# Kernel tuning notes

Measured on AMD Instinct MI355X. Metric: run time of the kernel, lower is better.

The kernel has to match this reference:

```python
import jax, jax.numpy as jnp
import numpy as np

B, T, I, H = 256, 512, 300, 128


def setup_inputs() -> dict:
    key = jax.random.key(0)
    ks = jax.random.split(key, 7)
    s_ih = 1.0 / np.sqrt(H)
    return {
        "x": jax.random.normal(ks[0], (B, T, I), dtype=jnp.float32),
        # PyTorch LSTM params, gate order i,f,g,o stacked along first axis
        "W_ih": jax.random.uniform(ks[1], (4 * H, I), minval=-s_ih, maxval=s_ih, dtype=jnp.float32),
        "W_hh": jax.random.uniform(ks[2], (4 * H, H), minval=-s_ih, maxval=s_ih, dtype=jnp.float32),
        "b_ih": jax.random.uniform(ks[3], (4 * H,), minval=-s_ih, maxval=s_ih, dtype=jnp.float32),
        "b_hh": jax.random.uniform(ks[4], (4 * H,), minval=-s_ih, maxval=s_ih, dtype=jnp.float32),
        "fc_w": jax.random.uniform(ks[5], (1, H), minval=-s_ih, maxval=s_ih, dtype=jnp.float32),
        "fc_b": jax.random.uniform(ks[6], (1,), minval=-s_ih, maxval=s_ih, dtype=jnp.float32),
    }


def _lstm_last_h(x, W_ih, W_hh, b_ih, b_hh):
    # Precompute input contributions for all timesteps at once: [B,T,4H]
    xg = jnp.einsum("bti,gi->btg", x, W_ih) + b_ih + b_hh
    xg = jnp.transpose(xg, (1, 0, 2))  # [T,B,4H] for scan

    def step(carry, xg_t):
        h, c = carry
        gates = xg_t + h @ W_hh.T  # [B,4H]
        i, f, g, o = jnp.split(gates, 4, axis=-1)
        i = jax.nn.sigmoid(i)
        f = jax.nn.sigmoid(f)
        g = jnp.tanh(g)
        o = jax.nn.sigmoid(o)
        c = f * c + i * g
        h = o * jnp.tanh(c)
        return (h, c), None

    h0 = jnp.zeros((x.shape[0], W_hh.shape[1]), dtype=x.dtype)
    (h_last, _), _ = jax.lax.scan(step, (h0, h0), xg)
    return h_last  # [B,H]


def reference(x, W_ih, W_hh, b_ih, b_hh, fc_w, fc_b):
    h_last = _lstm_last_h(x, W_ih, W_hh, b_ih, b_hh)
    return h_last @ fc_w.T + fc_b  # [B,1]
```

## Files before the change

kernel.cpp:

```cpp
#include <hip/hip_runtime.h>
#include <cstdint>
#include <cstddef>

#define Bb   256
#define Tt   512
#define Ii   300
#define Hh   128
#define G4   512
#define KP   320

typedef _Float16 h2v   __attribute__((ext_vector_type(2)));
typedef _Float16 half8 __attribute__((ext_vector_type(8)));
typedef float    f32x4 __attribute__((ext_vector_type(4)));

typedef __attribute__((address_space(3))) unsigned int lds_uint;
typedef const __attribute__((address_space(1))) unsigned int glb_uint;

static __device__ __forceinline__ h2v as_h2(unsigned int u){ union{unsigned int u; h2v h;} c; c.u=u; return c.h; }
static __device__ __forceinline__ unsigned int as_u32(h2v h){ union{unsigned int u; h2v h;} c; c.h=h; return c.u; }

#if __has_builtin(__builtin_amdgcn_fdot2)
#define FDOT2(a,b,c) __builtin_amdgcn_fdot2((a),(b),(c),false)
#else
static __device__ __forceinline__ float FDOT2(h2v a, h2v b, float c){
  return c + (float)a[0]*(float)b[0] + (float)a[1]*(float)b[1];
}
#endif

__global__ __launch_bounds__(256) void conv_x(const float* __restrict__ x, unsigned int* __restrict__ x16){
  int idx = blockIdx.x*256 + threadIdx.x;
  int r   = idx / 160;
  int kk2 = idx - r*160;
  int kk  = kk2*2;
  const float* xr = x + (size_t)r*Ii;
  float v0 = (kk   < Ii) ? xr[kk]   : 0.f;
  float v1 = (kk+1 < Ii) ? xr[kk+1] : 0.f;
  h2v h; h[0] = (_Float16)v0; h[1] = (_Float16)v1;
  x16[idx] = as_u32(h);
}

__global__ __launch_bounds__(256) void conv_small(const float* __restrict__ Wih, const float* __restrict__ Whh,
      const float* __restrict__ bih, const float* __restrict__ bhh,
      unsigned int* __restrict__ W16, unsigned int* __restrict__ Whh2, float* __restrict__ bias){
  int idx = blockIdx.x*256 + threadIdx.x;
  if (idx < G4*160){
    int r = idx/160, kk2 = idx - r*160, kk = kk2*2;
    const float* wr = Wih + (size_t)r*Ii;
    float v0 = (kk   < Ii) ? wr[kk]   : 0.f;
    float v1 = (kk+1 < Ii) ? wr[kk+1] : 0.f;
    h2v h; h[0]=(_Float16)v0; h[1]=(_Float16)v1;
    W16[idx] = as_u32(h);
  } else if (idx < G4*160 + G4*64){
    int t = idx - G4*160; int j = t>>6, kk = t&63;
    float v0 = Whh[j*Hh + kk*2], v1 = Whh[j*Hh + kk*2 + 1];
    h2v h; h[0]=(_Float16)v0; h[1]=(_Float16)v1;
    Whh2[t] = as_u32(h);
  } else if (idx < G4*160 + G4*64 + G4){
    int d = idx - (G4*160 + G4*64);
    bias[d] = bih[d] + bhh[d];
  }
}

__global__ __launch_bounds__(256,2) void gemm16(const _Float16* __restrict__ A, const _Float16* __restrict__ Bm,
       const float* __restrict__ bias, float* __restrict__ C){
  __shared__ __align__(16) _Float16 As[128*32];
  __shared__ __align__(16) _Float16 Bs[128*32];
  int tid = threadIdx.x;
  int w = tid>>6, lane = tid&63;
  int bm = blockIdx.x*128, bn = blockIdx.y*128;
  f32x4 acc[2][8];
  #pragma unroll
  for (int i=0;i<2;i++)
    #pragma unroll
    for (int j=0;j<8;j++) acc[i][j] = (f32x4){0.f,0.f,0.f,0.f};

  int L0 = w*128 + lane, L1 = L0 + 64;
  int r0 = L0>>2, c0 = (L0&3) ^ (r0&3);
  int r1 = L1>>2, c1 = (L1&3) ^ (r1&3);
  const _Float16* gA0 = A  + (size_t)(bm+r0)*KP + c0*8;
  const _Float16* gA1 = A  + (size_t)(bm+r1)*KP + c1*8;
  const _Float16* gB0 = Bm + (size_t)(bn+r0)*KP + c0*8;
  const _Float16* gB1 = Bm + (size_t)(bn+r1)*KP + c1*8;

  int q = lane>>4, mr = lane&15;
  int m0 = w*32;
  int ra0 = m0+mr, ra1 = m0+16+mr;
  int oa0 = ra0*32 + ((q ^ (ra0&3))*8);
  int oa1 = ra1*32 + ((q ^ (ra1&3))*8);
  int ob[8];
  #pragma unroll
  for (int j=0;j<8;j++){ int rb = j*16+mr; ob[j] = rb*32 + ((q ^ (rb&3))*8); }

  for (int kt=0; kt<KP/32; ++kt){
    __syncthreads();
    __builtin_amdgcn_global_load_lds((glb_uint*)gA0, (lds_uint*)&As[w*1024      ], 16, 0, 0);
    __builtin_amdgcn_global_load_lds((glb_uint*)gA1, (lds_uint*)&As[w*1024 + 512], 16, 0, 0);
    __builtin_amdgcn_global_load_lds((glb_uint*)gB0, (lds_uint*)&Bs[w*1024      ], 16, 0, 0);
    __builtin_amdgcn_global_load_lds((glb_uint*)gB1, (lds_uint*)&Bs[w*1024 + 512], 16, 0, 0);
    gA0 += 32; gA1 += 32; gB0 += 32; gB1 += 32;
    __syncthreads();
    half8 af0 = *(const half8*)&As[oa0];
    half8 af1 = *(const half8*)&As[oa1];
    #pragma unroll
    for (int j=0;j<8;j++){
      half8 bf = *(const half8*)&Bs[ob[j]];
      acc[0][j] = __builtin_amdgcn_mfma_f32_16x16x32_f16(af0, bf, acc[0][j], 0,0,0);
      acc[1][j] = __builtin_amdgcn_mfma_f32_16x16x32_f16(af1, bf, acc[1][j], 0,0,0);
    }
  }
  #pragma unroll
  for (int j=0;j<8;j++){
    int gc = bn + j*16 + mr;
    float bv = bias[gc];
    #pragma unroll
    for (int i=0;i<2;i++){
      int gr0 = bm + w*32 + i*16 + q*4;
      #pragma unroll
      for (int reg=0; reg<4; ++reg)
        C[(size_t)(gr0+reg)*G4 + gc] = acc[i][j][reg] + bv;
    }
  }
}

__global__ __launch_bounds__(512,2) void lstm_rec(const float* __restrict__ xg, const unsigned int* __restrict__ Whh2,
     const float* __restrict__ fcw, const float* __restrict__ fcb, float* __restrict__ out){
  int tid = threadIdx.x;
  int b = blockIdx.x;
  int d = tid & 127;
  h2v w[64];
  #pragma unroll
  for (int k=0; k<64; ++k) w[k] = as_h2(Whh2[tid*64 + k]);

  __shared__ __align__(16) unsigned short hsh[128];
  __shared__ float gsh[512];
  __shared__ __align__(16) float xbuf[2][16*G4];
  if (tid < 64) ((unsigned int*)hsh)[tid] = 0;

  const float* xrow = xg + (size_t)b * (Tt*G4);
  int wv = tid >> 6, lane = tid & 63;

  auto stage = [&](int c){
    const float* src = xrow + (size_t)c*16*G4;
    float* dst = xbuf[c & 1];
    #pragma unroll
    for (int i=0; i<4; ++i){
      int off = i*2048 + wv*256;
      __builtin_amdgcn_global_load_lds((glb_uint*)(src + off + lane*4),
                                       (lds_uint*)(dst + off), 16, 0, 0);
    }
  };

  stage(0);
  float creg = 0.f, hreg = 0.f;
  __syncthreads();

  for (int t=0; t<Tt; ++t){
    if ((t & 15) == 0){
      int nc = (t >> 4) + 1;
      if (nc < Tt/16) stage(nc);
    }
    float xv = xbuf[(t >> 4) & 1][(t & 15)*G4 + tid];
    float a0 = 0.f, a1 = 0.f;
    const uint4* hv = (const uint4*)hsh;
    #pragma unroll
    for (int kq=0; kq<8; ++kq){
      uint4 hq0 = hv[kq*2], hq1 = hv[kq*2+1];
      a0 = FDOT2(as_h2(hq0.x), w[kq*8+0], a0); a1 = FDOT2(as_h2(hq0.y), w[kq*8+1], a1);
      a0 = FDOT2(as_h2(hq0.z), w[kq*8+2], a0); a1 = FDOT2(as_h2(hq0.w), w[kq*8+3], a1);
      a0 = FDOT2(as_h2(hq1.x), w[kq*8+4], a0); a1 = FDOT2(as_h2(hq1.y), w[kq*8+5], a1);
      a0 = FDOT2(as_h2(hq1.z), w[kq*8+6], a0); a1 = FDOT2(as_h2(hq1.w), w[kq*8+7], a1);
    }
    float a = a0 + a1 + xv;
    float act;
    if ((tid >> 7) == 2){ float e = __expf(2.f*a); act = 1.f - 2.f/(e+1.f); }
    else                { act = 1.f/(1.f+__expf(-a)); }
    gsh[tid] = act;
    __syncthreads();
    float gi = gsh[d], gf = gsh[128+d], gg = gsh[256+d], go = gsh[384+d];
    creg = gf*creg + gi*gg;
    float ec = __expf(2.f*creg); float tc = 1.f - 2.f/(ec+1.f);
    hreg = go*tc;
    if (tid < 128){
      union{ _Float16 f; unsigned short u; } cv; cv.f = (_Float16)hreg;
      hsh[tid] = cv.u;
    }
    __syncthreads();
  }

  if (tid < 128) gsh[tid] = hreg * fcw[tid];
  __syncthreads();
  if (tid < 64){
    float s = gsh[tid] + gsh[tid+64];
    #pragma unroll
    for (int st=32; st>=1; st>>=1) s += __shfl_down(s, st, 64);
    if (tid == 0) out[b] = s + fcb[0];
  }
}

extern "C" void kernel_launch(void* const* d_in, const int* in_sizes, int n_in,
                              void* d_out, int out_size, void* d_ws, size_t ws_size,
                              hipStream_t stream){
  const float* x   = (const float*)d_in[0];
  const float* Wih = (const float*)d_in[1];
  const float* Whh = (const float*)d_in[2];
  const float* bih = (const float*)d_in[3];
  const float* bhh = (const float*)d_in[4];
  const float* fcw = (const float*)d_in[5];
  const float* fcb = (const float*)d_in[6];
  float* out = (float*)d_out;
  char* ws = (char*)d_ws;

  unsigned int* x16   = (unsigned int*)(ws);
  unsigned int* W16   = (unsigned int*)(ws + 83886080);
  unsigned int* Whh2w = (unsigned int*)(ws + 84213760);
  float*        bias  = (float*)      (ws + 84344832);
  float*        xg    = (float*)      (ws + 84346880);

  hipLaunchKernelGGL(conv_x,     dim3(81920),  dim3(256), 0, stream, x, x16);
  hipLaunchKernelGGL(conv_small, dim3(450),    dim3(256), 0, stream, Wih, Whh, bih, bhh, W16, Whh2w, bias);
  hipLaunchKernelGGL(gemm16,     dim3(1024,4), dim3(256), 0, stream,
                     (const _Float16*)x16, (const _Float16*)W16, bias, xg);
  hipLaunchKernelGGL(lstm_rec,   dim3(256),    dim3(512), 0, stream, xg, Whh2w, fcw, fcb, out);
}
```

Before: 723.7 us.

## Broadcast h via readlane and prefetch xg per step instead of LDS staging

Each lane now reads one packed pair of h from shared memory, and the full h vector is broadcast to the wave with readlane inside the recurrent dot product. This replaces the per-thread uint4 LDS reads of all of h. The double-buffered async LDS staging of xg chunks is replaced by a plain global load of the next timestep's value, issued one step ahead. The cell-state update is restricted to the first 128 threads. The aim is to cut LDS traffic and shared memory footprint on the serial critical path, at the cost of a global-load latency per step that must be hidden behind one iteration.

```diff
diff --git a/kernel.cpp b/kernel.cpp
--- a/kernel.cpp
+++ b/kernel.cpp
@@ -127,64 +127,48 @@
   int tid = threadIdx.x;
   int b = blockIdx.x;
   int d = tid & 127;
+  int lane = tid & 63;
   h2v w[64];
   #pragma unroll
   for (int k=0; k<64; ++k) w[k] = as_h2(Whh2[tid*64 + k]);
 
-  __shared__ __align__(16) unsigned short hsh[128];
+  __shared__ __align__(4) unsigned short hsh[128];
   __shared__ float gsh[512];
-  __shared__ __align__(16) float xbuf[2][16*G4];
   if (tid < 64) ((unsigned int*)hsh)[tid] = 0;
 
   const float* xrow = xg + (size_t)b * (Tt*G4);
-  int wv = tid >> 6, lane = tid & 63;
-
-  auto stage = [&](int c){
-    const float* src = xrow + (size_t)c*16*G4;
-    float* dst = xbuf[c & 1];
-    #pragma unroll
-    for (int i=0; i<4; ++i){
-      int off = i*2048 + wv*256;
-      __builtin_amdgcn_global_load_lds((glb_uint*)(src + off + lane*4),
-                                       (lds_uint*)(dst + off), 16, 0, 0);
-    }
-  };
-
-  stage(0);
+  float xc = xrow[tid];
   float creg = 0.f, hreg = 0.f;
   __syncthreads();
 
   for (int t=0; t<Tt; ++t){
-    if ((t & 15) == 0){
-      int nc = (t >> 4) + 1;
-      if (nc < Tt/16) stage(nc);
-    }
-    float xv = xbuf[(t >> 4) & 1][(t & 15)*G4 + tid];
-    float a0 = 0.f, a1 = 0.f;
-    const uint4* hv = (const uint4*)hsh;
-    #pragma unroll
-    for (int kq=0; kq<8; ++kq){
-      uint4 hq0 = hv[kq*2], hq1 = hv[kq*2+1];
-      a0 = FDOT2(as_h2(hq0.x), w[kq*8+0], a0); a1 = FDOT2(as_h2(hq0.y), w[kq*8+1], a1);
-      a0 = FDOT2(as_h2(hq0.z), w[kq*8+2], a0); a1 = FDOT2(as_h2(hq0.w), w[kq*8+3], a1);
-      a0 = FDOT2(as_h2(hq1.x), w[kq*8+4], a0); a1 = FDOT2(as_h2(hq1.y), w[kq*8+5], a1);
-      a0 = FDOT2(as_h2(hq1.z), w[kq*8+6], a0); a1 = FDOT2(as_h2(hq1.w), w[kq*8+7], a1);
-    }
-    float a = a0 + a1 + xv;
+    int tn = (t+1 < Tt) ? t+1 : t;
+    float xn = xrow[(size_t)tn*G4 + tid];
+    unsigned int hp = ((const unsigned int*)hsh)[lane];
+    float a0 = xc, a1 = 0.f;
+    #pragma unroll
+    for (int k=0; k<32; ++k){
+      unsigned int e0 = __builtin_amdgcn_readlane(hp, 2*k);
+      unsigned int e1 = __builtin_amdgcn_readlane(hp, 2*k+1);
+      a0 = FDOT2(as_h2(e0), w[2*k],   a0);
+      a1 = FDOT2(as_h2(e1), w[2*k+1], a1);
+    }
+    float a = a0 + a1;
     float act;
     if ((tid >> 7) == 2){ float e = __expf(2.f*a); act = 1.f - 2.f/(e+1.f); }
     else                { act = 1.f/(1.f+__expf(-a)); }
     gsh[tid] = act;
     __syncthreads();
-    float gi = gsh[d], gf = gsh[128+d], gg = gsh[256+d], go = gsh[384+d];
-    creg = gf*creg + gi*gg;
-    float ec = __expf(2.f*creg); float tc = 1.f - 2.f/(ec+1.f);
-    hreg = go*tc;
     if (tid < 128){
+      float gi = gsh[d], gf = gsh[128+d], gg = gsh[256+d], go = gsh[384+d];
+      creg = gf*creg + gi*gg;
+      float ec = __expf(2.f*creg); float tc = 1.f - 2.f/(ec+1.f);
+      hreg = go*tc;
       union{ _Float16 f; unsigned short u; } cv; cv.f = (_Float16)hreg;
       hsh[tid] = cv.u;
     }
     __syncthreads();
+    xc = xn;
   }
 
   if (tid < 128) gsh[tid] = hreg * fcw[tid];
```

Measured after the change: 754.0 us. 1.04x slower.
